# Kernel tuning notes

Measured on AMD Instinct MI355X. Metric: run time of the kernel, lower is better.

Reference implementation:

```python
import jax, jax.numpy as jnp
import numpy as np

B, T = 64, 1024
S, O = 512, 32000


def setup_inputs() -> dict:
    key = jax.random.key(0)
    k1, k2, k3, k4 = jax.random.split(key, 4)
    return {
        "observations": jax.random.randint(k1, (B, T), 0, O),
        "state_transitions": jax.random.normal(k2, (S, S), dtype=jnp.float32),
        "observation_transitions": jax.random.normal(k3, (S, O), dtype=jnp.float32),
        "prior_states": jax.random.normal(k4, (S,), dtype=jnp.float32),
    }


def reference(observations, state_transitions, observation_transitions, prior_states):
    # Precompute log-softmaxed parameters once (torch code recomputed per step).
    log_trans = jax.nn.log_softmax(state_transitions, axis=-1)        # [S, S]
    log_obs = jax.nn.log_softmax(observation_transitions, axis=-1)    # [S, O]
    log_prior = jax.nn.log_softmax(prior_states)                      # [S]

    b = observations.shape[0]
    # torch code appends a terminal observation 0 at the end of each sequence
    obs_seq = jnp.concatenate(
        [observations, jnp.zeros((b, 1), dtype=observations.dtype)], axis=1
    )  # [B, T+1]

    # alpha_0[b, s] = log_obs[s, o_0(b)] + log_prior[s]
    alpha0 = log_obs[:, obs_seq[:, 0]].T + log_prior  # [B, S]

    def step(alpha, obs_t):
        # alpha[b, i] -> pred[b, j] = logsumexp_i(alpha[b, i] + log_trans[i, j])
        pred = jax.nn.logsumexp(alpha[:, :, None] + log_trans[None, :, :], axis=1)  # [B, S]
        new_alpha = log_obs[:, obs_t].T + pred  # [B, S]
        return new_alpha, None

    alpha, _ = jax.lax.scan(step, alpha0, obs_seq[:, 1:].T)  # scan over T steps
    return jax.nn.logsumexp(alpha, axis=1)  # [B]
```

## Files before the change

kernel.cpp:

```cpp
#include <hip/hip_runtime.h>
#include <hip/hip_bf16.h>
#include <cstdint>

#define SS 512
#define OBS_N 32000
#define TT 1024
#define BB 64

#define RPW 24
#define TPW 8

typedef _Float16 h2 __attribute__((ext_vector_type(2)));

static __device__ __forceinline__ float wave_max(float v) {
#pragma unroll
  for (int m = 32; m >= 1; m >>= 1) v = fmaxf(v, __shfl_xor(v, m, 64));
  return v;
}
static __device__ __forceinline__ float wave_sum(float v) {
#pragma unroll
  for (int m = 32; m >= 1; m >>= 1) v += __shfl_xor(v, m, 64);
  return v;
}

static __device__ __forceinline__ float wave_max_dpp(float x) {
  int v = __builtin_bit_cast(int, x);
#define DPP_STEP(ctrl)                                                        \
  {                                                                           \
    int t = __builtin_amdgcn_update_dpp(v, v, (ctrl), 0xf, 0xf, false);       \
    v = __builtin_bit_cast(                                                   \
        int, fmaxf(__builtin_bit_cast(float, v), __builtin_bit_cast(float, t)));\
  }
  DPP_STEP(0x111)
  DPP_STEP(0x112)
  DPP_STEP(0x114)
  DPP_STEP(0x118)
  DPP_STEP(0x142)
  DPP_STEP(0x143)
#undef DPP_STEP
  return __builtin_bit_cast(float, __builtin_amdgcn_readlane(v, 63));
}

static __device__ __forceinline__ float dot2f(h2 a, h2 b, float c) {
#if __has_builtin(__builtin_amdgcn_fdot2)
  return __builtin_amdgcn_fdot2(a, b, c, false);
#else
  return c + (float)a.x * (float)b.x + (float)a.y * (float)b.y;
#endif
}

static __device__ __forceinline__ h2 as_h2(uint32_t u) {
  return __builtin_bit_cast(h2, u);
}
static __device__ __forceinline__ uint32_t sel4(const uint4& v, int s) {
  return s == 0 ? v.x : s == 1 ? v.y : s == 2 ? v.z : v.w;
}

__global__ __launch_bounds__(256) void prep_obs_lse(const float* __restrict__ ot,
                                                    float* __restrict__ lse) {
  const int s = blockIdx.x;
  const int tid = threadIdx.x;
  const float4* row = (const float4*)(ot + (size_t)s * OBS_N);
  __shared__ float redm[4];
  __shared__ float reds[4];

  float m = -INFINITY;
  for (int k = tid; k < OBS_N / 4; k += 256) {
    float4 v = row[k];
    m = fmaxf(m, fmaxf(fmaxf(v.x, v.y), fmaxf(v.z, v.w)));
  }
  m = wave_max(m);
  if ((tid & 63) == 0) redm[tid >> 6] = m;
  __syncthreads();
  m = fmaxf(fmaxf(redm[0], redm[1]), fmaxf(redm[2], redm[3]));

  float ssum = 0.f;
  for (int k = tid; k < OBS_N / 4; k += 256) {
    float4 v = row[k];
    ssum += __expf(v.x - m) + __expf(v.y - m) + __expf(v.z - m) + __expf(v.w - m);
  }
  ssum = wave_sum(ssum);
  if ((tid & 63) == 0) reds[tid >> 6] = ssum;
  __syncthreads();
  if (tid == 0) {
    float s4 = reds[0] + reds[1] + reds[2] + reds[3];
    lse[s] = m + __logf(s4);
  }
}

__global__ __launch_bounds__(512) void prep_trans(const float* __restrict__ st,
                                                  uint32_t* __restrict__ EP) {
  const int r = blockIdx.x;
  const int j = threadIdx.x;
  const int wv = j >> 6;
  float a0 = st[(size_t)(2 * r) * SS + j];
  float a1 = st[(size_t)(2 * r + 1) * SS + j];

  __shared__ float w0[8], w1[8], s0a[8], s1a[8];
  float m0 = wave_max(a0), m1 = wave_max(a1);
  if ((j & 63) == 0) { w0[wv] = m0; w1[wv] = m1; }
  __syncthreads();
  m0 = w0[0]; m1 = w1[0];
#pragma unroll
  for (int q = 1; q < 8; ++q) { m0 = fmaxf(m0, w0[q]); m1 = fmaxf(m1, w1[q]); }

  float e0 = __expf(a0 - m0), e1 = __expf(a1 - m1);
  float s0 = wave_sum(e0), s1 = wave_sum(e1);
  if ((j & 63) == 0) { s0a[wv] = s0; s1a[wv] = s1; }
  __syncthreads();
  s0 = 0.f; s1 = 0.f;
#pragma unroll
  for (int q = 0; q < 8; ++q) { s0 += s0a[q]; s1 += s1a[q]; }

  _Float16 h0 = (_Float16)(e0 / s0);
  _Float16 h1 = (_Float16)(e1 / s1);
  uint32_t u = ((uint32_t)__builtin_bit_cast(unsigned short, h1) << 16) |
               (uint32_t)__builtin_bit_cast(unsigned short, h0);
  EP[(size_t)r * SS + j] = u;
}

__global__ __launch_bounds__(512) void prep_prior(const float* __restrict__ pr,
                                                  float* __restrict__ lp) {
  const int j = threadIdx.x;
  const int wv = j >> 6;
  float a = pr[j];
  __shared__ float wm[8], ws[8];
  float m = wave_max(a);
  if ((j & 63) == 0) wm[wv] = m;
  __syncthreads();
  m = wm[0];
#pragma unroll
  for (int q = 1; q < 8; ++q) m = fmaxf(m, wm[q]);
  float e = __expf(a - m);
  float s = wave_sum(e);
  if ((j & 63) == 0) ws[wv] = s;
  __syncthreads();
  s = 0.f;
#pragma unroll
  for (int q = 0; q < 8; ++q) s += ws[q];
  lp[j] = a - m - __logf(s);
}

__global__ __launch_bounds__(512, 1) void hmm_main(
    const uint32_t* __restrict__ EP, const float* __restrict__ lse_obs,
    const float* __restrict__ lp, const int* __restrict__ obs,
    const float* __restrict__ ot, float* __restrict__ out) {
  __shared__ uint32_t eL[64][2][64][4];
  __shared__ __align__(16) unsigned short ph16[SS];
  __shared__ __align__(16) unsigned short ppb[2][8][SS];
  __shared__ __align__(16) float wred[2][8];
  __shared__ float fin_m[8], fin_s[8];

  const int tid = threadIdx.x;
  const int w = tid >> 6;
  const int l = tid & 63;
  const int b = blockIdx.x;
  const int j = tid;

  uint32_t eR[RPW * 8];
#pragma unroll
  for (int p = 0; p < RPW; ++p)
#pragma unroll
    for (int k = 0; k < 8; ++k)
      eR[p * 8 + k] = EP[(size_t)(32 * w + p) * SS + k * 64 + l];

  for (int idx = tid; idx < 64 * 2 * 64; idx += 512) {
    int tq = idx >> 7;
    int c = (idx >> 6) & 1;
    int ll = idx & 63;
    int pr = 32 * (tq >> 3) + RPW + (tq & 7);
    const uint32_t* src = EP + (size_t)pr * SS + c * 256 + ll;
    eL[tq][c][ll][0] = src[0];
    eL[tq][c][ll][1] = src[64];
    eL[tq][c][ll][2] = src[128];
    eL[tq][c][ll][3] = src[192];
  }

  const float lse_j = lse_obs[j];
  const float lpj = lp[j];
  const float* base_ot = ot + (size_t)j * OBS_N;
  const int* orow = obs + b * TT;

  const int o0 = orow[0];
  float alpha = base_ot[o0] - lse_j + lpj;

  int on = orow[1];
  float otv = base_ot[on];

  __syncthreads();

  for (int t = 1; t <= TT; ++t) {
    const int par = t & 1;

    int o2 = (t <= TT - 2) ? orow[t + 1] : 0;
    float ot_pf = (t < TT) ? base_ot[o2] : 0.f;

    float mw = wave_max_dpp(alpha);
    if (l == 0) wred[par][w] = mw;

    float Pj = __expf(alpha - mw);
    ph16[j] = __builtin_bit_cast(unsigned short, (_Float16)Pj);
    __builtin_amdgcn_wave_barrier();

    float acc[8] = {0.f, 0.f, 0.f, 0.f, 0.f, 0.f, 0.f, 0.f};

#pragma unroll
    for (int qg = 0; qg < 2; ++qg) {
      uint4 ph4 = *(const uint4*)&ph16[64 * w + 48 + 8 * qg];
#pragma unroll
      for (int s = 0; s < 4; ++s) {
        const int q = 4 * qg + s;
        h2 phv = as_h2(sel4(ph4, s));
        const uint4 c0 = *(const uint4*)&eL[w * 8 + q][0][l][0];
        const uint4 c1 = *(const uint4*)&eL[w * 8 + q][1][l][0];
        acc[0] = dot2f(phv, as_h2(c0.x), acc[0]);
        acc[1] = dot2f(phv, as_h2(c0.y), acc[1]);
        acc[2] = dot2f(phv, as_h2(c0.z), acc[2]);
        acc[3] = dot2f(phv, as_h2(c0.w), acc[3]);
        acc[4] = dot2f(phv, as_h2(c1.x), acc[4]);
        acc[5] = dot2f(phv, as_h2(c1.y), acc[5]);
        acc[6] = dot2f(phv, as_h2(c1.z), acc[6]);
        acc[7] = dot2f(phv, as_h2(c1.w), acc[7]);
      }
    }

#pragma unroll
    for (int g = 0; g < 6; ++g) {
      uint4 ph4 = *(const uint4*)&ph16[64 * w + 8 * g];
#pragma unroll
      for (int s = 0; s < 4; ++s) {
        const int p = 4 * g + s;
        h2 phv = as_h2(sel4(ph4, s));
#pragma unroll
        for (int k = 0; k < 8; ++k)
          acc[k] = dot2f(phv, as_h2(eR[p * 8 + k]), acc[k]);
      }
    }

#pragma unroll
    for (int k = 0; k < 8; ++k)
      ppb[par][w][k * 64 + l] =
          __builtin_bit_cast(unsigned short, (_Float16)acc[k]);

    __syncthreads();

    const float4 wv0 = *(const float4*)&wred[par][0];
    const float4 wv1 = *(const float4*)&wred[par][4];
    float M = fmaxf(fmaxf(fmaxf(wv0.x, wv0.y), fmaxf(wv0.z, wv0.w)),
                    fmaxf(fmaxf(wv1.x, wv1.y), fmaxf(wv1.z, wv1.w)));
    float earg = wred[par][l & 7];
    float ee = __expf(earg - M);

    float pred = 0.f;
#pragma unroll
    for (int q = 0; q < 8; ++q) {
      float eq = __builtin_bit_cast(
          float, __builtin_amdgcn_readlane(__builtin_bit_cast(int, ee), q));
      float pq = (float)__builtin_bit_cast(_Float16, ppb[par][q][j]);
      pred = fmaf(eq, pq, pred);
    }
    alpha = M + __logf(pred) + (otv - lse_j);
    otv = ot_pf;
  }

  float m = wave_max(alpha);
  if (l == 0) fin_m[w] = m;
  __syncthreads();
  float M = fin_m[0];
#pragma unroll
  for (int q = 1; q < 8; ++q) M = fmaxf(M, fin_m[q]);
  float e = __expf(alpha - M);
  float s = wave_sum(e);
  if (l == 0) fin_s[w] = s;
  __syncthreads();
  if (tid == 0) {
    float tot = 0.f;
#pragma unroll
    for (int q = 0; q < 8; ++q) tot += fin_s[q];
    out[b] = M + __logf(tot);
  }
}

extern "C" void kernel_launch(void* const* d_in, const int* in_sizes, int n_in,
                              void* d_out, int out_size, void* d_ws, size_t ws_size,
                              hipStream_t stream) {
  const int* obs = (const int*)d_in[0];
  const float* st = (const float*)d_in[1];
  const float* ot = (const float*)d_in[2];
  const float* pr = (const float*)d_in[3];
  float* out = (float*)d_out;

  char* ws = (char*)d_ws;
  uint32_t* EP = (uint32_t*)ws;
  float* lse_obs = (float*)(ws + 524288);
  float* lprior = (float*)(ws + 524288 + 2048);

  prep_obs_lse<<<SS, 256, 0, stream>>>(ot, lse_obs);
  prep_trans<<<SS / 2, SS, 0, stream>>>(st, EP);
  prep_prior<<<1, SS, 0, stream>>>(pr, lprior);
  hmm_main<<<BB, SS, 0, stream>>>(EP, lse_obs, lprior, obs, ot, out);
}
```

Before: 1.864 ms.

## Transpose observation matrix so per-step emission gathers are coalesced

Adds a tiled transpose kernel that writes observation_transitions as [O, S] into the workspace when it is large enough. The main kernel then reads emission values with stride parameters, so the 512 threads of a block load one contiguous row per timestep instead of 512 scattered, strided addresses. The cost is an extra 64 MB read and write pass per call, plus a fallback to the old layout when the workspace is too small. It also replaces the occupancy hint with amdgpu_waves_per_eu(2,2).

```diff
diff --git a/kernel.cpp b/kernel.cpp
--- a/kernel.cpp
+++ b/kernel.cpp
@@ -88,6 +88,22 @@
   }
 }
 
+__global__ __launch_bounds__(256) void transpose_ot(const float* __restrict__ ot,
+                                                    float* __restrict__ oT) {
+  __shared__ float tile[32][33];
+  const int o0 = blockIdx.x * 32;
+  const int j0 = blockIdx.y * 32;
+  const int tx = threadIdx.x & 31;
+  const int ty = threadIdx.x >> 5;
+#pragma unroll
+  for (int r = 0; r < 32; r += 8)
+    tile[ty + r][tx] = ot[(size_t)(j0 + ty + r) * OBS_N + (o0 + tx)];
+  __syncthreads();
+#pragma unroll
+  for (int r = 0; r < 32; r += 8)
+    oT[(size_t)(o0 + ty + r) * SS + (j0 + tx)] = tile[tx][ty + r];
+}
+
 __global__ __launch_bounds__(512) void prep_trans(const float* __restrict__ st,
                                                   uint32_t* __restrict__ EP) {
   const int r = blockIdx.x;
@@ -141,10 +157,11 @@
   lp[j] = a - m - __logf(s);
 }
 
-__global__ __launch_bounds__(512, 1) void hmm_main(
+__attribute__((amdgpu_waves_per_eu(2, 2))) __global__ void
+__launch_bounds__(512) hmm_main(
     const uint32_t* __restrict__ EP, const float* __restrict__ lse_obs,
     const float* __restrict__ lp, const int* __restrict__ obs,
-    const float* __restrict__ ot, float* __restrict__ out) {
+    const float* __restrict__ og, int sO, int sJ, float* __restrict__ out) {
   __shared__ uint32_t eL[64][2][64][4];
   __shared__ __align__(16) unsigned short ph16[SS];
   __shared__ __align__(16) unsigned short ppb[2][8][SS];
@@ -178,14 +195,14 @@
 
   const float lse_j = lse_obs[j];
   const float lpj = lp[j];
-  const float* base_ot = ot + (size_t)j * OBS_N;
+  const size_t jOff = (size_t)j * sJ;
   const int* orow = obs + b * TT;
 
   const int o0 = orow[0];
-  float alpha = base_ot[o0] - lse_j + lpj;
+  float alpha = og[(size_t)o0 * sO + jOff] - lse_j + lpj;
 
   int on = orow[1];
-  float otv = base_ot[on];
+  float otv = og[(size_t)on * sO + jOff];
 
   __syncthreads();
 
@@ -193,7 +210,7 @@
     const int par = t & 1;
 
     int o2 = (t <= TT - 2) ? orow[t + 1] : 0;
-    float ot_pf = (t < TT) ? base_ot[o2] : 0.f;
+    float ot_pf = (t < TT) ? og[(size_t)o2 * sO + jOff] : 0.f;
 
     float mw = wave_max_dpp(alpha);
     if (l == 0) wred[par][w] = mw;
@@ -293,10 +310,19 @@
   char* ws = (char*)d_ws;
   uint32_t* EP = (uint32_t*)ws;
   float* lse_obs = (float*)(ws + 524288);
-  float* lprior = (float*)(ws + 524288 + 2048);
+  float* lprior = (float*)(ws + 526336);
+  float* oT = (float*)(ws + 528384);
+  const size_t need = 528384 + (size_t)OBS_N * SS * sizeof(float);
 
   prep_obs_lse<<<SS, 256, 0, stream>>>(ot, lse_obs);
   prep_trans<<<SS / 2, SS, 0, stream>>>(st, EP);
   prep_prior<<<1, SS, 0, stream>>>(pr, lprior);
-  hmm_main<<<BB, SS, 0, stream>>>(EP, lse_obs, lprior, obs, ot, out);
-}
+
+  const float* og = ot;
+  int sO = 1, sJ = OBS_N;
+  if (ws_size >= need) {
+    transpose_ot<<<dim3(OBS_N / 32, SS / 32), 256, 0, stream>>>(ot, oT);
+    og = oT; sO = SS; sJ = 1;
+  }
+  hmm_main<<<BB, SS, 0, stream>>>(EP, lse_obs, lprior, obs, og, sO, sJ, out);
+}
```

After: 1.861 ms. Within noise of the previous version (-0.2%).
